# Optimization experiments

Hardware: AMD Instinct MI355X
Metric: run time of the kernel (lower is better)

Reference implementation:

```python
import jax, jax.numpy as jnp
import numpy as np

B, S, HID = 4, 1024, 1024
NH, HD = 16, 64  # num heads, head dim


def setup_inputs() -> dict:
    key = jax.random.key(0)
    ks = jax.random.split(key, 8)
    scale = 0.02
    return {
        "hidden_states": jax.random.normal(ks[0], (B, S, HID), dtype=jnp.float32),
        "attention_mask": jnp.ones((B, 1, 1, S), dtype=jnp.float32),
        "Wq": jax.random.normal(ks[1], (HID, HID), dtype=jnp.float32) * scale,
        "bq": jnp.zeros((HID,), dtype=jnp.float32),
        "Wk": jax.random.normal(ks[2], (HID, HID), dtype=jnp.float32) * scale,
        "bk": jnp.zeros((HID,), dtype=jnp.float32),
        "Wv": jax.random.normal(ks[3], (HID, HID), dtype=jnp.float32) * scale,
        "bv": jnp.zeros((HID,), dtype=jnp.float32),
    }


def reference(hidden_states, attention_mask, Wq, bq, Wk, bk, Wv, bv):
    # Linear projections: torch nn.Linear computes x @ W.T + b
    q = hidden_states @ Wq.T + bq  # [B,S,HID]
    k = hidden_states @ Wk.T + bk
    v = hidden_states @ Wv.T + bv

    def split_heads(x):
        return x.reshape(B, S, NH, HD).transpose(0, 2, 1, 3)  # [B,NH,S,HD]

    q, k, v = split_heads(q), split_heads(k), split_heads(v)

    scores = jnp.einsum("bhqd,bhkd->bhqk", q, k) / jnp.sqrt(jnp.float32(HD))
    # faithful to original: scores - (2 - mask) * 1e6
    scores = scores - (2.0 - attention_mask) * 1.0e6
    probs = jax.nn.softmax(scores, axis=-1)
    # dropout: eval mode -> identity
    ctx = jnp.einsum("bhqk,bhkd->bhqd", probs, v)  # [B,NH,S,HD]
    ctx = ctx.transpose(0, 2, 1, 3).reshape(B, S, HID)
    return ctx
```

## Files before the change

kernel.cpp:

```cpp
#include <hip/hip_runtime.h>
#include <math.h>

#define B_ 4
#define S_ 1024
#define HID_ 1024
#define NH_ 16
#define HD_ 64
#define NTOK (B_ * S_)

typedef __attribute__((ext_vector_type(4))) float f32x4;
typedef __attribute__((ext_vector_type(16))) float f32x16;
typedef __attribute__((ext_vector_type(8))) short bf16x8;

__device__ __forceinline__ unsigned short f2bf(float f) {
    union { float f; unsigned int u; } v; v.f = f;
    unsigned int r = v.u + 0x7fffu + ((v.u >> 16) & 1u);
    return (unsigned short)(r >> 16);
}

#if __has_builtin(__builtin_amdgcn_cvt_pk_bf16_f32)
__device__ __forceinline__ unsigned int pk_bf16(float a, float b) {
    auto v = __builtin_amdgcn_cvt_pk_bf16_f32(a, b);
    union { decltype(v) v; unsigned int u; } cv; cv.v = v;
    return cv.u;
}
#else
__device__ __forceinline__ unsigned int pk_bf16(float a, float b) {
    return (unsigned int)f2bf(a) | ((unsigned int)f2bf(b) << 16);
}
#endif

#if __has_builtin(__builtin_amdgcn_permlane32_swap)
__device__ __forceinline__ void plswap(unsigned &a, unsigned &b) {
    typedef __attribute__((ext_vector_type(2))) int v2i;
    v2i r = __builtin_amdgcn_permlane32_swap((int)a, (int)b, false, false);
    a = (unsigned)r[0]; b = (unsigned)r[1];
}
#else
__device__ __forceinline__ void plswap(unsigned &a, unsigned &b) {
    const unsigned bl = __shfl_xor(b, 32);
    const unsigned ah = __shfl_xor(a, 32);
    const bool hi = ((threadIdx.x & 63) >> 5) != 0;
    const unsigned na = hi ? bl : a;
    const unsigned nb = hi ? b  : ah;
    a = na; b = nb;
}
#endif

__device__ __forceinline__ void load_lds16(const void* g, void* l) {
    __builtin_amdgcn_global_load_lds(
        (const __attribute__((address_space(1))) unsigned int*)(uintptr_t)g,
        (__attribute__((address_space(3))) unsigned int*)(uintptr_t)l,
        16, 0, 0);
}

__global__ __launch_bounds__(256) void cvt_all(
    const float* __restrict__ x, const float* __restrict__ wq,
    const float* __restrict__ wk, const float* __restrict__ wv,
    unsigned short* __restrict__ xb, unsigned short* __restrict__ wqb,
    unsigned short* __restrict__ wkb, unsigned short* __restrict__ wvb)
{
    const int which = blockIdx.y;
    const float* src = which == 0 ? x : which == 1 ? wq : which == 2 ? wk : wv;
    unsigned short* dst = which == 0 ? xb : which == 1 ? wqb : which == 2 ? wkb : wvb;
    const int n4 = (which == 0) ? (NTOK * HID_ / 4) : (HID_ * HID_ / 4);
    int i = blockIdx.x * 256 + threadIdx.x;
    if (i < n4) {
        float4 f = ((const float4*)src)[i];
        uint2 o;
        o.x = pk_bf16(f.x, f.y);
        o.y = pk_bf16(f.z, f.w);
        ((uint2*)dst)[i] = o;
    }
}

__global__ __launch_bounds__(512, 2) void qkv_gemm_mfma(
    const unsigned short* __restrict__ xb,
    const unsigned short* __restrict__ Wqb, const float* __restrict__ bq,
    const unsigned short* __restrict__ Wkb, const float* __restrict__ bk,
    const unsigned short* __restrict__ Wvb, const float* __restrict__ bv,
    unsigned short* __restrict__ qout, unsigned short* __restrict__ kout,
    unsigned short* __restrict__ vtout)
{
    extern __shared__ char sm[];

    const int which = blockIdx.z;
    const unsigned short* __restrict__ W = which == 0 ? Wqb : which == 1 ? Wkb : Wvb;
    const float* __restrict__ bias       = which == 0 ? bq  : which == 1 ? bk  : bv;

    const int t    = threadIdx.x;
    const int lane = t & 63;
    const int w    = t >> 6;
    const int wr   = w >> 2;
    const int wc   = w & 3;
    const int g    = lane >> 4;
    const int lrow = lane & 15;

    const unsigned short* __restrict__ Arow = (which == 2) ? W  : xb;
    const unsigned short* __restrict__ Brow = (which == 2) ? xb : W;
    const int am0 = (which == 2) ? blockIdx.y * 256 : blockIdx.x * 256;
    const int bn0 = (which == 2) ? blockIdx.x * 256 : blockIdx.y * 256;

    const int r0  = t >> 2;
    const int c0  = t & 3;
    const int csw = (c0 ^ ((r0 >> 1) & 3)) << 3;
    const unsigned short* gA = Arow + (size_t)(am0 + r0) * HID_ + csw;
    const unsigned short* gB = Brow + (size_t)(bn0 + r0) * HID_ + csw;

    const int sw4  = (g ^ ((lrow >> 1) & 3)) << 4;
    const int aoff = wr * 8192 + lrow * 64 + sw4;
    const int boff = wc * 4096 + lrow * 64 + sw4;

    f32x4 acc[8][4];
    #pragma unroll
    for (int m = 0; m < 8; ++m)
        #pragma unroll
        for (int n = 0; n < 4; ++n) acc[m][n] = (f32x4){0.f, 0.f, 0.f, 0.f};

    auto stageA = [&](int kt) {
        char* dst = sm + (kt & 3) * 32768;
        const unsigned short* s = gA + kt * 32;
        load_lds16(s, dst + t * 16);
        load_lds16(s + (size_t)128 * HID_, dst + 8192 + t * 16);
    };
    auto stageB = [&](int kt) {
        char* dst = sm + (kt & 3) * 32768 + 16384;
        const unsigned short* s = gB + kt * 32;
        load_lds16(s, dst + t * 16);
        load_lds16(s + (size_t)128 * HID_, dst + 8192 + t * 16);
    };

    stageA(0); stageB(0); stageA(1); stageB(1); stageA(2); stageB(2);
    asm volatile("s_waitcnt vmcnt(8)" ::: "memory");
    asm volatile("s_barrier" ::: "memory");

    for (int kt = 0; kt < 32; ++kt) {
        const char* Ab = sm + (kt & 3) * 32768;
        const char* Bb = Ab + 16384;

        if (kt < 29) { stageA(kt + 3); stageB(kt + 3); }

        bf16x8 af[8], bf[4];
        #pragma unroll
        for (int m = 0; m < 8; ++m) af[m] = *(const bf16x8*)(Ab + aoff + m * 1024);
        #pragma unroll
        for (int n = 0; n < 4; ++n) bf[n] = *(const bf16x8*)(Bb + boff + n * 1024);
        __builtin_amdgcn_s_setprio(1);
        #pragma unroll
        for (int m = 0; m < 8; ++m)
            #pragma unroll
            for (int n = 0; n < 4; ++n)
                acc[m][n] = __builtin_amdgcn_mfma_f32_16x16x32_bf16(
                    af[m], bf[n], acc[m][n], 0, 0, 0);
        __builtin_amdgcn_s_setprio(0);

        if (kt <= 28) {
            asm volatile("s_waitcnt vmcnt(8)" ::: "memory");
        } else if (kt == 29) {
            asm volatile("s_waitcnt vmcnt(4)" ::: "memory");
        } else if (kt == 30) {
            asm volatile("s_waitcnt vmcnt(0)" ::: "memory");
        }
        asm volatile("s_barrier" ::: "memory");
    }

    const int col   = lane & 15;
    const int rbase = (lane >> 4) << 2;
    if (which == 2) {
        #pragma unroll
        for (int m = 0; m < 8; ++m) {
            #pragma unroll
            for (int rr = 0; rr < 4; ++rr) {
                const int feat = am0 + wr * 128 + m * 16 + rbase + rr;
                const int h = feat >> 6, d = feat & 63;
                const float bias_v = bias[feat];
                #pragma unroll
                for (int n = 0; n < 4; ++n) {
                    const int tok = bn0 + wc * 64 + n * 16 + col;
                    const int b = tok >> 10, s = tok & 1023;
                    vtout[((size_t)((b << 4) + h) << 16) + ((size_t)d << 10) + s] =
                        f2bf(acc[m][n][rr] + bias_v);
                }
            }
        }
    } else {
        #pragma unroll
        for (int n = 0; n < 4; ++n) {
            const int feat = bn0 + wc * 64 + n * 16 + col;
            const int h = feat >> 6, d = feat & 63;
            const float bias_v = bias[feat];
            #pragma unroll
            for (int m = 0; m < 8; ++m) {
                #pragma unroll
                for (int rr = 0; rr < 4; ++rr) {
                    const int tok = am0 + wr * 128 + m * 16 + rbase + rr;
                    const int b = tok >> 10, s = tok & 1023;
                    const size_t off = ((size_t)((b << 4) + h) << 16) + ((size_t)s << 6) + d;
                    const float val = acc[m][n][rr] + bias_v;
                    if (which == 0) qout[off] = f2bf(val);
                    else            kout[off] = f2bf(val);
                }
            }
        }
    }
}

__global__ __launch_bounds__(512, 4) void attn_mfma(
    const unsigned short* __restrict__ Q, const unsigned short* __restrict__ K,
    const unsigned short* __restrict__ Vt, const float* __restrict__ mask,
    float* __restrict__ out)
{
    __shared__ unsigned short Ks[2][2][64 * 64];
    __shared__ unsigned short Vts[2][64 * 64];
    __shared__ float Mts[1024];

    const int t    = threadIdx.x;
    const int lane = t & 63;
    const int w    = t >> 6;
    const int kh   = w >> 2;
    const int pw   = w & 3;
    const int q31  = lane & 31;
    const int hl   = lane >> 5;

    const int bh = blockIdx.x;
    const int b  = bh >> 4;
    const int h  = bh & 15;
    const int q0w = (blockIdx.y << 7) + (pw << 5);

    const unsigned short* __restrict__ qg = Q  + ((size_t)bh << 16);
    const unsigned short* __restrict__ kg = K  + ((size_t)bh << 16);
    const unsigned short* __restrict__ vg = Vt + ((size_t)bh << 16);

    bf16x8 qreg[4];
    {
        const unsigned short* qp = qg + ((size_t)(q0w + q31) << 6);
        #pragma unroll
        for (int kc = 0; kc < 4; ++kc)
            qreg[kc] = *(const bf16x8*)&qp[kc * 16 + (hl << 3)];
    }

    int fro[4];
    #pragma unroll
    for (int kc = 0; kc < 4; ++kc)
        fro[kc] = q31 * 128 + ((((kc << 1) + hl) ^ (q31 & 7)) << 4);

    const int srow = t >> 3;
    const int c8   = ((t & 7) ^ (srow & 7)) << 3;
    const unsigned short* kstat = kg + (size_t)srow * 64 + c8;
    const unsigned short* vstat = vg + (size_t)srow * 1024 + c8;

    f32x16 O[2];
    #pragma unroll
    for (int i = 0; i < 16; ++i) { O[0][i] = 0.f; O[1][i] = 0.f; }
    float lacc = 0.f;

    #pragma unroll
    for (int hh = 0; hh < 2; ++hh)
        load_lds16(kstat + hh * 32768, (char*)Ks[hh][0] + t * 16);
    #pragma unroll
    for (int i = 0; i < 2; ++i) {
        const int key = t + i * 512;
        Mts[key] = (2.0f - mask[(b << 10) + key]) * 1.0e6f;
    }
    __syncthreads();

    for (int kt = 0; kt < 8; ++kt) {
        const int cur = kt & 1;

        #pragma unroll
        for (int hh = 0; hh < 2; ++hh) {
            load_lds16(vstat + hh * 512 + (size_t)kt * 64, (char*)Vts[hh] + t * 16);
            if (kt < 7)
                load_lds16(kstat + hh * 32768 + (size_t)(kt + 1) * 4096,
                           (char*)Ks[hh][cur ^ 1] + t * 16);
        }

        const char* Kb = (const char*)Ks[kh][cur];
        const char* Vb = (const char*)Vts[kh];

        f32x16 sacc[2];
        #pragma unroll
        for (int i = 0; i < 16; ++i) { sacc[0][i] = 0.f; sacc[1][i] = 0.f; }
        #pragma unroll
        for (int kb = 0; kb < 2; ++kb) {
            bf16x8 kf[4];
            #pragma unroll
            for (int kc = 0; kc < 4; ++kc)
                kf[kc] = *(const bf16x8*)(Kb + kb * 4096 + fro[kc]);
            __builtin_amdgcn_s_setprio(1);
            #pragma unroll
            for (int kc = 0; kc < 4; ++kc)
                sacc[kb] = __builtin_amdgcn_mfma_f32_32x32x16_bf16(
                    kf[kc], qreg[kc], sacc[kb], 0, 0, 0);
            __builtin_amdgcn_s_setprio(0);
        }

        bf16x8 pf[4];
        #pragma unroll
        for (int kb = 0; kb < 2; ++kb) {
            unsigned u[4][2];
            #pragma unroll
            for (int rq = 0; rq < 4; ++rq) {
                const f32x4 m4 = *(const f32x4*)&Mts[(kh << 9) + kt * 64 + kb * 32 + rq * 8 + (hl << 2)];
                float p[4];
                #pragma unroll
                for (int r = 0; r < 4; ++r) {
                    const float sv = sacc[kb][rq * 4 + r] * 0.125f - m4[r];
                    p[r] = __expf(sv + 1.0e6f);
                }
                lacc += (p[0] + p[1]) + (p[2] + p[3]);
                u[rq][0] = pk_bf16(p[0], p[1]);
                u[rq][1] = pk_bf16(p[2], p[3]);
            }
            #pragma unroll
            for (int c = 0; c < 2; ++c) {
                unsigned w0 = u[2 * c][0], w2 = u[2 * c + 1][0];
                plswap(w0, w2);
                unsigned w1 = u[2 * c][1], w3 = u[2 * c + 1][1];
                plswap(w1, w3);
                union { unsigned uu[4]; bf16x8 v; } f;
                f.uu[0] = w0; f.uu[1] = w1; f.uu[2] = w2; f.uu[3] = w3;
                pf[kb * 2 + c] = f.v;
            }
        }

        __syncthreads();

        #pragma unroll
        for (int hb = 0; hb < 2; ++hb) {
            bf16x8 vf[4];
            #pragma unroll
            for (int kc = 0; kc < 4; ++kc)
                vf[kc] = *(const bf16x8*)(Vb + hb * 4096 + fro[kc]);
            __builtin_amdgcn_s_setprio(1);
            #pragma unroll
            for (int kc = 0; kc < 4; ++kc)
                O[hb] = __builtin_amdgcn_mfma_f32_32x32x16_bf16(
                    pf[kc], vf[kc], O[hb], 0, 0, 0);
            __builtin_amdgcn_s_setprio(0);
        }

        __syncthreads();
    }

    float* Osh = (float*)&Ks[0][0][0];
    float* Lsh = (float*)&Vts[0][0];
    const float l = lacc + __shfl_xor(lacc, 32);
    if (kh == 1) {
        #pragma unroll
        for (int r = 0; r < 16; ++r) {
            const int qr = (r & 3) + ((r >> 2) << 3) + (hl << 2);
            Osh[pw * 2048 + qr * 64 + q31]      = O[0][r];
            Osh[pw * 2048 + qr * 64 + 32 + q31] = O[1][r];
        }
        if (lane < 32) Lsh[pw * 32 + q31] = l;
    } else {
        if (lane < 32) Lsh[128 + pw * 32 + q31] = l;
    }
    __syncthreads();
    if (kh == 0) {
        #pragma unroll
        for (int r = 0; r < 16; ++r) {
            const int qr = (r & 3) + ((r >> 2) << 3) + (hl << 2);
            const float inv = 1.0f / (Lsh[128 + pw * 32 + qr] + Lsh[pw * 32 + qr]);
            const size_t base = (((size_t)(b << 10) + (q0w + qr)) << 10) + (h << 6);
            out[base + q31]      = (O[0][r] + Osh[pw * 2048 + qr * 64 + q31])      * inv;
            out[base + 32 + q31] = (O[1][r] + Osh[pw * 2048 + qr * 64 + 32 + q31]) * inv;
        }
    }
}

extern "C" void kernel_launch(void* const* d_in, const int* in_sizes, int n_in,
                              void* d_out, int out_size, void* d_ws, size_t ws_size,
                              hipStream_t stream) {
    const float* hs   = (const float*)d_in[0];
    const float* mask = (const float*)d_in[1];
    const float* Wq   = (const float*)d_in[2];
    const float* bq   = (const float*)d_in[3];
    const float* Wk   = (const float*)d_in[4];
    const float* bk   = (const float*)d_in[5];
    const float* Wv   = (const float*)d_in[6];
    const float* bv   = (const float*)d_in[7];
    float* out = (float*)d_out;

    char* ws = (char*)d_ws;
    unsigned short* xb  = (unsigned short*)(ws);
    unsigned short* wqb = (unsigned short*)(ws + ((size_t)8  << 20));
    unsigned short* wkb = (unsigned short*)(ws + ((size_t)10 << 20));
    unsigned short* wvb = (unsigned short*)(ws + ((size_t)12 << 20));
    unsigned short* qb  = (unsigned short*)(ws + ((size_t)14 << 20));
    unsigned short* kb  = (unsigned short*)(ws + ((size_t)22 << 20));
    unsigned short* vtb = (unsigned short*)(ws + ((size_t)30 << 20));

    static bool attr_set = false;
    if (!attr_set) {
        hipFuncSetAttribute((const void*)qkv_gemm_mfma,
                            hipFuncAttributeMaxDynamicSharedMemorySize, 131072);
        attr_set = true;
    }

    cvt_all<<<dim3(4096, 4), 256, 0, stream>>>(hs, Wq, Wk, Wv, xb, wqb, wkb, wvb);
    qkv_gemm_mfma<<<dim3(NTOK / 256, HID_ / 256, 3), 512, 131072, stream>>>(
        xb, wqb, bq, wkb, bk, wvb, bv, qb, kb, vtb);
    attn_mfma<<<dim3(B_ * NH_, S_ / 128), 512, 0, stream>>>(qb, kb, vtb, mask, out);
}
```

Measured before the change: 152.7 us.

## Shrink QKV GEMM tile to 256x128 with 3-stage pipeline for more blocks

Shrinks the QKV projection GEMM block tile from 256x256 to 256x128. The 8 waves move from a 2x4 to a 4x2 layout, each holding 4x4 accumulators. The LDS ring drops from a 4-stage, 3-deep prefetch (128KB) to a 3-stage, 2-deep prefetch (72KB), and the grid is flattened to 128x3 blocks with launch bounds raised to 4. The aim is to double the block count (384 vs 192) and raise occupancy so the 256 CUs are better filled. In exchange, each block does less data reuse per load and has a shallower prefetch pipeline.

```diff
diff --git a/kernel.cpp b/kernel.cpp
--- a/kernel.cpp
+++ b/kernel.cpp
@@ -74,7 +74,7 @@
     }
 }
 
-__global__ __launch_bounds__(512, 2) void qkv_gemm_mfma(
+__global__ __launch_bounds__(512, 4) void qkv_gemm_mfma(
     const unsigned short* __restrict__ xb,
     const unsigned short* __restrict__ Wqb, const float* __restrict__ bq,
     const unsigned short* __restrict__ Wkb, const float* __restrict__ bk,
@@ -84,22 +84,25 @@
 {
     extern __shared__ char sm[];
 
-    const int which = blockIdx.z;
+    const int which = blockIdx.y;
     const unsigned short* __restrict__ W = which == 0 ? Wqb : which == 1 ? Wkb : Wvb;
     const float* __restrict__ bias       = which == 0 ? bq  : which == 1 ? bk  : bv;
 
     const int t    = threadIdx.x;
     const int lane = t & 63;
     const int w    = t >> 6;
-    const int wr   = w >> 2;
-    const int wc   = w & 3;
+    const int wm   = w >> 1;
+    const int wn   = w & 1;
     const int g    = lane >> 4;
     const int lrow = lane & 15;
 
     const unsigned short* __restrict__ Arow = (which == 2) ? W  : xb;
     const unsigned short* __restrict__ Brow = (which == 2) ? xb : W;
-    const int am0 = (which == 2) ? blockIdx.y * 256 : blockIdx.x * 256;
-    const int bn0 = (which == 2) ? blockIdx.x * 256 : blockIdx.y * 256;
+    const int bx  = blockIdx.x;
+    const int bm  = (which == 2) ? (bx >> 5) : (bx >> 3);
+    const int bnn = (which == 2) ? (bx & 31) : (bx & 7);
+    const int am0 = bm * 256;
+    const int bn0 = bnn * 128;
 
     const int r0  = t >> 2;
     const int c0  = t & 3;
@@ -108,56 +111,49 @@
     const unsigned short* gB = Brow + (size_t)(bn0 + r0) * HID_ + csw;
 
     const int sw4  = (g ^ ((lrow >> 1) & 3)) << 4;
-    const int aoff = wr * 8192 + lrow * 64 + sw4;
-    const int boff = wc * 4096 + lrow * 64 + sw4;
-
-    f32x4 acc[8][4];
+    const int aoff = wm * 4096 + lrow * 64 + sw4;
+    const int boff = wn * 4096 + lrow * 64 + sw4;
+
+    f32x4 acc[4][4];
     #pragma unroll
-    for (int m = 0; m < 8; ++m)
+    for (int m = 0; m < 4; ++m)
         #pragma unroll
         for (int n = 0; n < 4; ++n) acc[m][n] = (f32x4){0.f, 0.f, 0.f, 0.f};
 
-    auto stageA = [&](int kt) {
-        char* dst = sm + (kt & 3) * 32768;
-        const unsigned short* s = gA + kt * 32;
-        load_lds16(s, dst + t * 16);
-        load_lds16(s + (size_t)128 * HID_, dst + 8192 + t * 16);
+    auto stage = [&](int kt) {
+        char* dst = sm + (kt % 3) * 24576;
+        const unsigned short* sa = gA + kt * 32;
+        load_lds16(sa, dst + t * 16);
+        load_lds16(sa + (size_t)128 * HID_, dst + 8192 + t * 16);
+        load_lds16(gB + kt * 32, dst + 16384 + t * 16);
     };
-    auto stageB = [&](int kt) {
-        char* dst = sm + (kt & 3) * 32768 + 16384;
-        const unsigned short* s = gB + kt * 32;
-        load_lds16(s, dst + t * 16);
-        load_lds16(s + (size_t)128 * HID_, dst + 8192 + t * 16);
-    };
-
-    stageA(0); stageB(0); stageA(1); stageB(1); stageA(2); stageB(2);
-    asm volatile("s_waitcnt vmcnt(8)" ::: "memory");
+
+    stage(0); stage(1);
+    asm volatile("s_waitcnt vmcnt(3)" ::: "memory");
     asm volatile("s_barrier" ::: "memory");
 
     for (int kt = 0; kt < 32; ++kt) {
-        const char* Ab = sm + (kt & 3) * 32768;
+        const char* Ab = sm + (kt % 3) * 24576;
         const char* Bb = Ab + 16384;
 
-        if (kt < 29) { stageA(kt + 3); stageB(kt + 3); }
-
-        bf16x8 af[8], bf[4];
-        #pragma unroll
-        for (int m = 0; m < 8; ++m) af[m] = *(const bf16x8*)(Ab + aoff + m * 1024);
+        if (kt < 30) stage(kt + 2);
+
+        bf16x8 af[4], bf[4];
+        #pragma unroll
+        for (int m = 0; m < 4; ++m) af[m] = *(const bf16x8*)(Ab + aoff + m * 1024);
         #pragma unroll
         for (int n = 0; n < 4; ++n) bf[n] = *(const bf16x8*)(Bb + boff + n * 1024);
         __builtin_amdgcn_s_setprio(1);
         #pragma unroll
-        for (int m = 0; m < 8; ++m)
+        for (int m = 0; m < 4; ++m)
             #pragma unroll
             for (int n = 0; n < 4; ++n)
                 acc[m][n] = __builtin_amdgcn_mfma_f32_16x16x32_bf16(
                     af[m], bf[n], acc[m][n], 0, 0, 0);
         __builtin_amdgcn_s_setprio(0);
 
-        if (kt <= 28) {
-            asm volatile("s_waitcnt vmcnt(8)" ::: "memory");
-        } else if (kt == 29) {
-            asm volatile("s_waitcnt vmcnt(4)" ::: "memory");
+        if (kt <= 29) {
+            asm volatile("s_waitcnt vmcnt(3)" ::: "memory");
         } else if (kt == 30) {
             asm volatile("s_waitcnt vmcnt(0)" ::: "memory");
         }
@@ -168,15 +164,15 @@
     const int rbase = (lane >> 4) << 2;
     if (which == 2) {
         #pragma unroll
-        for (int m = 0; m < 8; ++m) {
+        for (int m = 0; m < 4; ++m) {
             #pragma unroll
             for (int rr = 0; rr < 4; ++rr) {
-                const int feat = am0 + wr * 128 + m * 16 + rbase + rr;
+                const int feat = am0 + wm * 64 + m * 16 + rbase + rr;
                 const int h = feat >> 6, d = feat & 63;
                 const float bias_v = bias[feat];
                 #pragma unroll
                 for (int n = 0; n < 4; ++n) {
-                    const int tok = bn0 + wc * 64 + n * 16 + col;
+                    const int tok = bn0 + wn * 64 + n * 16 + col;
                     const int b = tok >> 10, s = tok & 1023;
                     vtout[((size_t)((b << 4) + h) << 16) + ((size_t)d << 10) + s] =
                         f2bf(acc[m][n][rr] + bias_v);
@@ -186,14 +182,14 @@
     } else {
         #pragma unroll
         for (int n = 0; n < 4; ++n) {
-            const int feat = bn0 + wc * 64 + n * 16 + col;
+            const int feat = bn0 + wn * 64 + n * 16 + col;
             const int h = feat >> 6, d = feat & 63;
             const float bias_v = bias[feat];
             #pragma unroll
-            for (int m = 0; m < 8; ++m) {
+            for (int m = 0; m < 4; ++m) {
                 #pragma unroll
                 for (int rr = 0; rr < 4; ++rr) {
-                    const int tok = am0 + wr * 128 + m * 16 + rbase + rr;
+                    const int tok = am0 + wm * 64 + m * 16 + rbase + rr;
                     const int b = tok >> 10, s = tok & 1023;
                     const size_t off = ((size_t)((b << 4) + h) << 16) + ((size_t)s << 6) + d;
                     const float val = acc[m][n][rr] + bias_v;
@@ -400,7 +396,7 @@
     }
 
     cvt_all<<<dim3(4096, 4), 256, 0, stream>>>(hs, Wq, Wk, Wv, xb, wqb, wkb, wvb);
-    qkv_gemm_mfma<<<dim3(NTOK / 256, HID_ / 256, 3), 512, 131072, stream>>>(
+    qkv_gemm_mfma<<<dim3(128, 3), 512, 73728, stream>>>(
         xb, wqb, bq, wkb, bk, wvb, bv, qb, kb, vtb);
     attn_mfma<<<dim3(B_ * NH_, S_ / 128), 512, 0, stream>>>(qb, kb, vtb, mask, out);
 }
```

Result: no change. 152.4 us (-0.2%).
